# Performance work log

Hardware: AMD Instinct MI355X
Metric: run time of the kernel (lower is better)

The kernel has to match this reference:

```python
import jax, jax.numpy as jnp
import numpy as np

B, N, M, K = 8, 24000, 6000, 32
C_IN, C_MID, C_OUT = 64, 128, 256  # channels=[64,128,256]; conv input is C_IN+3 (dp_fj)


def setup_inputs() -> dict:
    key = jax.random.key(0)
    ks = jax.random.split(key, 8)
    return {
        "query_xyz": jax.random.normal(ks[0], (B, M, 3), jnp.float32),
        "support_xyz": jax.random.normal(ks[1], (B, N, 3), jnp.float32),
        "features": jax.random.normal(ks[2], (B, C_IN, N), jnp.float32),
        "neighbor_idx": jax.random.randint(ks[3], (B, M, K), 0, N, dtype=jnp.int32),
        "W1": jax.random.normal(ks[4], (C_MID, C_IN + 3), jnp.float32) * 0.05,
        "b1": jnp.zeros((C_MID,), jnp.float32),
        "W2": jax.random.normal(ks[5], (C_OUT, C_MID), jnp.float32) * 0.05,
        "b2": jnp.zeros((C_OUT,), jnp.float32),
    }


def _conv1d_relu(x, W, b):
    # pointwise conv1d (kernel size 1) + bias + ReLU; x: [B, Cin, N]
    return jax.nn.relu(jnp.einsum('oc,bcn->bon', W, x) + b[None, :, None])


def reference(query_xyz, support_xyz, features, neighbor_idx, W1, b1, W2, b2):
    # Delayed aggregation: transform features FIRST (convs on support points),
    # then gather neighbors per query and max-reduce.
    x = jnp.concatenate([features, support_xyz.transpose(0, 2, 1)], axis=1)  # [B, C_IN+3, N]
    x = _conv1d_relu(x, W1, b1)   # [B, C_MID, N]
    x = _conv1d_relu(x, W2, b2)   # [B, C_OUT, N]
    # grouper: gather neighbor features fj = x[b, :, neighbor_idx[b, m, k]] -> [B, C_OUT, M, K]
    idx = jnp.broadcast_to(neighbor_idx.reshape(B, 1, M * K), (B, C_OUT, M * K))
    fj = jnp.take_along_axis(x, idx, axis=2).reshape(B, C_OUT, M, K)
    # reduction_layer: max over neighbor dim
    return jnp.max(fj, axis=-1)  # [B, C_OUT, M]
```

## Files before the change

### kernel.cpp

```cpp
#include <hip/hip_runtime.h>

typedef unsigned short u16;
typedef short s16x8 __attribute__((ext_vector_type(8)));
typedef float f32x4 __attribute__((ext_vector_type(4)));

#define B_   8
#define N_   24000
#define M_   6000
#define K_   32
#define CIN  64
#define CMID 128
#define COUT 256
#define KP1  96

__device__ __align__(16) u16 g_W1p[CMID * KP1];
__device__ __align__(16) u16 g_W2b[COUT * CMID];
__device__ __align__(16) u16 g_Yf[(size_t)B_ * N_ * COUT];

__device__ __forceinline__ float bf2f(u16 u) {
    return __uint_as_float(((unsigned)u) << 16);
}
__device__ __forceinline__ u16 f2bf(float f) {
    unsigned u = __float_as_uint(f);
    u += 0x7FFFu + ((u >> 16) & 1u);
    return (u16)(u >> 16);
}

__global__ void prep_weights(const float* __restrict__ W1,
                             const float* __restrict__ W2) {
    int t = blockIdx.x * 256 + threadIdx.x;
    if (t < CMID * KP1) {
        int m = t / KP1, k = t % KP1;
        g_W1p[t] = (k < 67) ? f2bf(W1[m * 67 + k]) : (u16)0;
    } else {
        int i = t - CMID * KP1;
        g_W2b[i] = f2bf(W2[i]);
    }
}

__global__ __launch_bounds__(256) void conv_fused(
        const float* __restrict__ feat, const float* __restrict__ xyz,
        const float* __restrict__ b1,  const float* __restrict__ b2) {
    __shared__ __align__(16) u16 sm[16896];
    u16* Xs = sm;
    u16* Hs = sm + 6656;
    u16* Ys = sm;

    const int tid  = threadIdx.x;
    const int b    = blockIdx.y;
    const int n0   = blockIdx.x * 64;
    const int w    = tid >> 6;
    const int L    = tid & 63;
    const int ln   = L & 15;
    const int quad = L >> 4;

    if (tid < 64) {
        uint4 z; z.x = z.y = z.z = z.w = 0u;
        u16* xr = Xs + tid * 104;
        *(uint4*)(xr + 64) = z; *(uint4*)(xr + 72) = z;
        *(uint4*)(xr + 80) = z; *(uint4*)(xr + 88) = z;
        const float* s = xyz + (size_t)(b * N_ + n0 + tid) * 3;
        xr[64] = f2bf(s[0]); xr[65] = f2bf(s[1]); xr[66] = f2bf(s[2]);
    }
#pragma unroll
    for (int it = 0; it < 4; ++it) {
        int idx = it * 256 + tid;
        int c   = idx >> 4;
        int p0  = (idx & 15) << 2;
        float4 v = *(const float4*)(feat + (size_t)(b * CIN + c) * N_ + n0 + p0);
        u16* dst = Xs + p0 * 104 + c;
        dst[0]   = f2bf(v.x);
        dst[104] = f2bf(v.y);
        dst[208] = f2bf(v.z);
        dst[312] = f2bf(v.w);
    }
    __syncthreads();

    f32x4 acc1[2][4];
#pragma unroll
    for (int mt = 0; mt < 2; ++mt)
#pragma unroll
        for (int nt = 0; nt < 4; ++nt) {
            f32x4 zz = {0.f, 0.f, 0.f, 0.f};
            acc1[mt][nt] = zz;
        }
#pragma unroll
    for (int k0 = 0; k0 < KP1; k0 += 32) {
        s16x8 af[2], bf[4];
#pragma unroll
        for (int mt = 0; mt < 2; ++mt)
            af[mt] = *(const s16x8*)(g_W1p + (size_t)(w * 32 + mt * 16 + ln) * KP1 + k0 + quad * 8);
#pragma unroll
        for (int nt = 0; nt < 4; ++nt)
            bf[nt] = *(const s16x8*)(Xs + (nt * 16 + ln) * 104 + k0 + quad * 8);
#pragma unroll
        for (int mt = 0; mt < 2; ++mt)
#pragma unroll
            for (int nt = 0; nt < 4; ++nt)
                acc1[mt][nt] = __builtin_amdgcn_mfma_f32_16x16x32_bf16(
                    af[mt], bf[nt], acc1[mt][nt], 0, 0, 0);
    }
#pragma unroll
    for (int mt = 0; mt < 2; ++mt) {
        int m0 = w * 32 + mt * 16 + quad * 4;
        float4 bv = *(const float4*)(b1 + m0);
#pragma unroll
        for (int nt = 0; nt < 4; ++nt) {
            int p = nt * 16 + ln;
            float x0 = acc1[mt][nt][0] + bv.x;
            float x1 = acc1[mt][nt][1] + bv.y;
            float x2 = acc1[mt][nt][2] + bv.z;
            float x3 = acc1[mt][nt][3] + bv.w;
            ushort4 hv;
            hv.x = f2bf(x0 > 0.f ? x0 : 0.f);
            hv.y = f2bf(x1 > 0.f ? x1 : 0.f);
            hv.z = f2bf(x2 > 0.f ? x2 : 0.f);
            hv.w = f2bf(x3 > 0.f ? x3 : 0.f);
            *(ushort4*)(Hs + p * 136 + m0) = hv;
        }
    }
    __syncthreads();

    f32x4 acc2[4][4];
#pragma unroll
    for (int mt = 0; mt < 4; ++mt)
#pragma unroll
        for (int nt = 0; nt < 4; ++nt) {
            f32x4 zz = {0.f, 0.f, 0.f, 0.f};
            acc2[mt][nt] = zz;
        }
#pragma unroll
    for (int k0 = 0; k0 < CMID; k0 += 32) {
        s16x8 af[4], bf[4];
#pragma unroll
        for (int mt = 0; mt < 4; ++mt)
            af[mt] = *(const s16x8*)(g_W2b + (size_t)(w * 64 + mt * 16 + ln) * CMID + k0 + quad * 8);
#pragma unroll
        for (int nt = 0; nt < 4; ++nt)
            bf[nt] = *(const s16x8*)(Hs + (nt * 16 + ln) * 136 + k0 + quad * 8);
#pragma unroll
        for (int mt = 0; mt < 4; ++mt)
#pragma unroll
            for (int nt = 0; nt < 4; ++nt)
                acc2[mt][nt] = __builtin_amdgcn_mfma_f32_16x16x32_bf16(
                    af[mt], bf[nt], acc2[mt][nt], 0, 0, 0);
    }
    __syncthreads();

#pragma unroll
    for (int mt = 0; mt < 4; ++mt) {
        int c0 = w * 64 + mt * 16 + quad * 4;
        float4 bv = *(const float4*)(b2 + c0);
#pragma unroll
        for (int nt = 0; nt < 4; ++nt) {
            int p = nt * 16 + ln;
            float x0 = acc2[mt][nt][0] + bv.x;
            float x1 = acc2[mt][nt][1] + bv.y;
            float x2 = acc2[mt][nt][2] + bv.z;
            float x3 = acc2[mt][nt][3] + bv.w;
            ushort4 yv;
            yv.x = f2bf(x0 > 0.f ? x0 : 0.f);
            yv.y = f2bf(x1 > 0.f ? x1 : 0.f);
            yv.z = f2bf(x2 > 0.f ? x2 : 0.f);
            yv.w = f2bf(x3 > 0.f ? x3 : 0.f);
            *(ushort4*)(Ys + p * 264 + c0) = yv;
        }
    }
    __syncthreads();

    u16* dstY = g_Yf + ((size_t)b * N_ + n0) * COUT;
#pragma unroll
    for (int i = 0; i < 8; ++i) {
        int g = i * 256 + tid;
        int p = g >> 5, c16 = g & 31;
        *(uint4*)(dstY + (size_t)p * COUT + c16 * 8) =
            *(const uint4*)(Ys + p * 264 + c16 * 8);
    }
}

__global__ __launch_bounds__(256) void gather_max(
        const int* __restrict__ nbr, float* __restrict__ out) {
    __shared__ __align__(16) int sidx[64 * K_];
    __shared__ __align__(16) u16 ymax[COUT * 68];

    const int tid = threadIdx.x;
    const int b   = blockIdx.y;
    const int m0  = blockIdx.x * 64;

#pragma unroll
    for (int it = 0; it < 2; ++it) {
        int g = it * 256 + tid;
        if (m0 + (g >> 3) < M_)
            *(int4*)(sidx + g * 4) =
                *(const int4*)(nbr + (size_t)(b * M_ + m0) * K_ + g * 4);
    }
    __syncthreads();

    const int w = tid >> 6, L = tid & 63;
    const u16* base = g_Yf + (size_t)b * N_ * COUT + L * 4;
    for (int i = 0; i < 16; ++i) {
        int ml = w * 16 + i;
        if (m0 + ml >= M_) break;
        ushort4 mx; mx.x = 0; mx.y = 0; mx.z = 0; mx.w = 0;
#pragma unroll
        for (int k = 0; k < K_; ++k) {
            int idx = __builtin_amdgcn_readfirstlane(sidx[ml * K_ + k]);
            idx = ((unsigned)idx < (unsigned)N_) ? idx : 0;
            ushort4 v = *(const ushort4*)(base + (size_t)idx * COUT);
            mx.x = v.x > mx.x ? v.x : mx.x;
            mx.y = v.y > mx.y ? v.y : mx.y;
            mx.z = v.z > mx.z ? v.z : mx.z;
            mx.w = v.w > mx.w ? v.w : mx.w;
        }
        u16* yp = ymax + (L * 4) * 68 + ml;
        yp[0] = mx.x; yp[68] = mx.y; yp[136] = mx.z; yp[204] = mx.w;
    }
    __syncthreads();

    int valid = M_ - m0; if (valid > 64) valid = 64;
#pragma unroll
    for (int i = 0; i < 8; ++i) {
        int c  = i * 32 + (tid >> 3);
        int mc = (tid & 7) << 3;
        if (mc + 8 <= valid) {
            const u16* src = ymax + c * 68 + mc;
            float4 v0, v1;
            v0.x = bf2f(src[0]); v0.y = bf2f(src[1]);
            v0.z = bf2f(src[2]); v0.w = bf2f(src[3]);
            v1.x = bf2f(src[4]); v1.y = bf2f(src[5]);
            v1.z = bf2f(src[6]); v1.w = bf2f(src[7]);
            float* dst = out + (size_t)(b * COUT + c) * M_ + m0 + mc;
            *(float4*)dst       = v0;
            *(float4*)(dst + 4) = v1;
        }
    }
}

extern "C" void kernel_launch(void* const* d_in, const int* in_sizes, int n_in,
                              void* d_out, int out_size, void* d_ws, size_t ws_size,
                              hipStream_t stream) {
    const float* xyz  = (const float*)d_in[1];
    const float* feat = (const float*)d_in[2];
    const int*   nbr  = (const int*)d_in[3];
    const float* W1   = (const float*)d_in[4];
    const float* b1   = (const float*)d_in[5];
    const float* W2   = (const float*)d_in[6];
    const float* b2   = (const float*)d_in[7];
    float* out = (float*)d_out;
    (void)d_ws; (void)ws_size;

    prep_weights<<<176, 256, 0, stream>>>(W1, W2);
    conv_fused<<<dim3(N_ / 64, B_), 256, 0, stream>>>(feat, xyz, b1, b2);
    gather_max<<<dim3((M_ + 63) / 64, B_), 256, 0, stream>>>(nbr, out);
}
```

Measured before the change: 296.3 us.

## Pre-swizzle weights into MFMA fragment order and halve gather tile size

```diff
diff --git a/kernel.cpp b/kernel.cpp
--- a/kernel.cpp
+++ b/kernel.cpp
@@ -13,8 +13,8 @@
 #define COUT 256
 #define KP1  96
 
-__device__ __align__(16) u16 g_W1p[CMID * KP1];
-__device__ __align__(16) u16 g_W2b[COUT * CMID];
+__device__ __align__(16) u16 g_W1f[CMID * KP1];
+__device__ __align__(16) u16 g_W2f[COUT * CMID];
 __device__ __align__(16) u16 g_Yf[(size_t)B_ * N_ * COUT];
 
 __device__ __forceinline__ float bf2f(u16 u) {
@@ -30,11 +30,24 @@
                              const float* __restrict__ W2) {
     int t = blockIdx.x * 256 + threadIdx.x;
     if (t < CMID * KP1) {
-        int m = t / KP1, k = t % KP1;
-        g_W1p[t] = (k < 67) ? f2bf(W1[m * 67 + k]) : (u16)0;
+        int blk = t >> 9, off = t & 511;
+        int L = off >> 3, j = off & 7;
+        int ln = L & 15, quad = L >> 4;
+        int w = blk / 6, r = blk % 6;
+        int k0i = r >> 1, mt = r & 1;
+        int row = w * 32 + mt * 16 + ln;
+        int col = k0i * 32 + quad * 8 + j;
+        g_W1f[t] = (col < 67) ? f2bf(W1[row * 67 + col]) : (u16)0;
     } else {
         int i = t - CMID * KP1;
-        g_W2b[i] = f2bf(W2[i]);
+        int blk = i >> 9, off = i & 511;
+        int L = off >> 3, j = off & 7;
+        int ln = L & 15, quad = L >> 4;
+        int w = blk >> 4, r = blk & 15;
+        int k0i = r >> 2, mt = r & 3;
+        int row = w * 64 + mt * 16 + ln;
+        int col = k0i * 32 + quad * 8 + j;
+        g_W2f[i] = f2bf(W2[row * 128 + col]);
     }
 }
 
@@ -85,20 +98,20 @@
             acc1[mt][nt] = zz;
         }
 #pragma unroll
-    for (int k0 = 0; k0 < KP1; k0 += 32) {
-        s16x8 af[2], bf[4];
+    for (int k0i = 0; k0i < 3; ++k0i) {
+        s16x8 af[2], xf[4];
 #pragma unroll
         for (int mt = 0; mt < 2; ++mt)
-            af[mt] = *(const s16x8*)(g_W1p + (size_t)(w * 32 + mt * 16 + ln) * KP1 + k0 + quad * 8);
+            af[mt] = *(const s16x8*)(g_W1f + (((w * 3 + k0i) * 2 + mt) << 9) + L * 8);
 #pragma unroll
         for (int nt = 0; nt < 4; ++nt)
-            bf[nt] = *(const s16x8*)(Xs + (nt * 16 + ln) * 104 + k0 + quad * 8);
+            xf[nt] = *(const s16x8*)(Xs + (nt * 16 + ln) * 104 + k0i * 32 + quad * 8);
 #pragma unroll
         for (int mt = 0; mt < 2; ++mt)
 #pragma unroll
             for (int nt = 0; nt < 4; ++nt)
                 acc1[mt][nt] = __builtin_amdgcn_mfma_f32_16x16x32_bf16(
-                    af[mt], bf[nt], acc1[mt][nt], 0, 0, 0);
+                    af[mt], xf[nt], acc1[mt][nt], 0, 0, 0);
     }
 #pragma unroll
     for (int mt = 0; mt < 2; ++mt) {
@@ -130,20 +143,20 @@
             acc2[mt][nt] = zz;
         }
 #pragma unroll
-    for (int k0 = 0; k0 < CMID; k0 += 32) {
-        s16x8 af[4], bf[4];
+    for (int k0i = 0; k0i < 4; ++k0i) {
+        s16x8 af[4], hf[4];
 #pragma unroll
         for (int mt = 0; mt < 4; ++mt)
-            af[mt] = *(const s16x8*)(g_W2b + (size_t)(w * 64 + mt * 16 + ln) * CMID + k0 + quad * 8);
+            af[mt] = *(const s16x8*)(g_W2f + (((w * 4 + k0i) * 4 + mt) << 9) + L * 8);
 #pragma unroll
         for (int nt = 0; nt < 4; ++nt)
-            bf[nt] = *(const s16x8*)(Hs + (nt * 16 + ln) * 136 + k0 + quad * 8);
+            hf[nt] = *(const s16x8*)(Hs + (nt * 16 + ln) * 136 + k0i * 32 + quad * 8);
 #pragma unroll
         for (int mt = 0; mt < 4; ++mt)
 #pragma unroll
             for (int nt = 0; nt < 4; ++nt)
                 acc2[mt][nt] = __builtin_amdgcn_mfma_f32_16x16x32_bf16(
-                    af[mt], bf[nt], acc2[mt][nt], 0, 0, 0);
+                    af[mt], hf[nt], acc2[mt][nt], 0, 0, 0);
     }
     __syncthreads();
 
@@ -180,26 +193,23 @@
 
 __global__ __launch_bounds__(256) void gather_max(
         const int* __restrict__ nbr, float* __restrict__ out) {
-    __shared__ __align__(16) int sidx[64 * K_];
-    __shared__ __align__(16) u16 ymax[COUT * 68];
+    __shared__ __align__(16) int sidx[32 * K_];
+    __shared__ __align__(16) u16 ymax[COUT * 36];
 
     const int tid = threadIdx.x;
     const int b   = blockIdx.y;
-    const int m0  = blockIdx.x * 64;
-
-#pragma unroll
-    for (int it = 0; it < 2; ++it) {
-        int g = it * 256 + tid;
-        if (m0 + (g >> 3) < M_)
-            *(int4*)(sidx + g * 4) =
-                *(const int4*)(nbr + (size_t)(b * M_ + m0) * K_ + g * 4);
-    }
+    const int m0  = blockIdx.x * 32;
+
+    if (m0 + (tid >> 3) < M_)
+        *(int4*)(sidx + tid * 4) =
+            *(const int4*)(nbr + ((size_t)b * M_ + m0) * K_ + tid * 4);
     __syncthreads();
 
     const int w = tid >> 6, L = tid & 63;
     const u16* base = g_Yf + (size_t)b * N_ * COUT + L * 4;
-    for (int i = 0; i < 16; ++i) {
-        int ml = w * 16 + i;
+#pragma unroll
+    for (int i = 0; i < 8; ++i) {
+        int ml = w * 8 + i;
         if (m0 + ml >= M_) break;
         ushort4 mx; mx.x = 0; mx.y = 0; mx.z = 0; mx.w = 0;
 #pragma unroll
@@ -212,26 +222,22 @@
             mx.z = v.z > mx.z ? v.z : mx.z;
             mx.w = v.w > mx.w ? v.w : mx.w;
         }
-        u16* yp = ymax + (L * 4) * 68 + ml;
-        yp[0] = mx.x; yp[68] = mx.y; yp[136] = mx.z; yp[204] = mx.w;
-    }
-    __syncthreads();
-
-    int valid = M_ - m0; if (valid > 64) valid = 64;
+        u16* yp = ymax + (L * 4) * 36 + ml;
+        yp[0] = mx.x; yp[36] = mx.y; yp[72] = mx.z; yp[108] = mx.w;
+    }
+    __syncthreads();
+
+    int valid = M_ - m0; if (valid > 32) valid = 32;
 #pragma unroll
     for (int i = 0; i < 8; ++i) {
         int c  = i * 32 + (tid >> 3);
-        int mc = (tid & 7) << 3;
-        if (mc + 8 <= valid) {
-            const u16* src = ymax + c * 68 + mc;
-            float4 v0, v1;
-            v0.x = bf2f(src[0]); v0.y = bf2f(src[1]);
-            v0.z = bf2f(src[2]); v0.w = bf2f(src[3]);
-            v1.x = bf2f(src[4]); v1.y = bf2f(src[5]);
-            v1.z = bf2f(src[6]); v1.w = bf2f(src[7]);
-            float* dst = out + (size_t)(b * COUT + c) * M_ + m0 + mc;
-            *(float4*)dst       = v0;
-            *(float4*)(dst + 4) = v1;
+        int mc = (tid & 7) << 2;
+        if (mc + 4 <= valid) {
+            const u16* src = ymax + c * 36 + mc;
+            float4 v;
+            v.x = bf2f(src[0]); v.y = bf2f(src[1]);
+            v.z = bf2f(src[2]); v.w = bf2f(src[3]);
+            *(float4*)(out + (size_t)(b * COUT + c) * M_ + m0 + mc) = v;
         }
     }
 }
@@ -251,5 +257,5 @@
 
     prep_weights<<<176, 256, 0, stream>>>(W1, W2);
     conv_fused<<<dim3(N_ / 64, B_), 256, 0, stream>>>(feat, xyz, b1, b2);
-    gather_max<<<dim3((M_ + 63) / 64, B_), 256, 0, stream>>>(nbr, out);
-}
+    gather_max<<<dim3((M_ + 31) / 32, B_), 256, 0, stream>>>(nbr, out);
+}
```

Measured after the change: 282.8 us. -4.6%, faster.
